# Performance work log

Measured on AMD Instinct MI355X. Metric: run time of the kernel, lower is better.

The kernel has to match this reference:

```python
import jax, jax.numpy as jnp
import numpy as np

N_NODES = 100000
N_EDGES = 1600000
HEADS = 8
CH = 16
NEG_SLOPE = 0.2


def setup_inputs() -> dict:
    key = jax.random.key(0)
    ks = jax.random.split(key, 8)
    x = jax.random.normal(ks[0], (N_NODES, 16), dtype=jnp.float32)
    edge_index = jax.random.randint(ks[1], (2, N_EDGES), 0, N_NODES, dtype=jnp.int64)
    W = jax.random.normal(ks[2], (16, HEADS * CH), dtype=jnp.float32) * 0.25
    att_src = jax.random.normal(ks[3], (HEADS, CH), dtype=jnp.float32) * 0.25
    att_dst = jax.random.normal(ks[4], (HEADS, CH), dtype=jnp.float32) * 0.25
    bias = jax.random.normal(ks[5], (HEADS * CH,), dtype=jnp.float32) * 0.1
    fc_w = jax.random.normal(ks[6], (HEADS * CH, 5), dtype=jnp.float32) * 0.1
    fc_b = jax.random.normal(ks[7], (5,), dtype=jnp.float32) * 0.1
    return {"x": x, "edge_index": edge_index, "W": W, "att_src": att_src,
            "att_dst": att_dst, "bias": bias, "fc_w": fc_w, "fc_b": fc_b}


def reference(x, edge_index, W, att_src, att_dst, bias, fc_w, fc_b):
    N = x.shape[0]
    # PyG GATConv default: add self loops
    loops = jnp.arange(N, dtype=edge_index.dtype)
    src = jnp.concatenate([edge_index[0], loops])
    dst = jnp.concatenate([edge_index[1], loops])

    h = (x @ W).reshape(N, HEADS, CH)                 # [N,H,C]
    a_src = jnp.einsum('nhc,hc->nh', h, att_src)      # [N,H]
    a_dst = jnp.einsum('nhc,hc->nh', h, att_dst)      # [N,H]

    e = a_src[src] + a_dst[dst]                       # [E,H]
    e = jax.nn.leaky_relu(e, NEG_SLOPE)
    # segment softmax over edges grouped by destination node
    e_max = jax.ops.segment_max(e, dst, num_segments=N)
    e_exp = jnp.exp(e - e_max[dst])
    denom = jax.ops.segment_sum(e_exp, dst, num_segments=N)
    alpha = e_exp / (denom[dst] + 1e-16)              # [E,H]

    msg = alpha[:, :, None] * h[src]                  # [E,H,C]
    out = jax.ops.segment_sum(msg, dst, num_segments=N)  # [N,H,C]
    out = out.reshape(N, HEADS * CH) + bias           # concat heads + bias

    out = jax.nn.relu(out)
    # dropout is identity in eval mode
    logits = out @ fc_w + fc_b                        # [N,5]
    return jax.nn.log_softmax(logits, axis=1)
```

## Files before the change

kernel.cpp:

```cpp
#include <hip/hip_runtime.h>
#include <hip/hip_bf16.h>
#include <hip/hip_fp16.h>
#include <math.h>

#define N_NODES 100000
#define N_EDGES 1600000
#define HEADS 8
#define HC 128
#define LOG2E 1.44269504f

#define DPB 64
#define NB 1563
#define NBP (NB + 1)
#define NCH 512
#define EPC (N_EDGES / NCH)
#define CAPS 1664
#define WSTR (CAPS + 4)
#define NA 196

__global__ __launch_bounds__(512) void k_prep(
    const float* __restrict__ x, const float* __restrict__ W,
    const float* __restrict__ att_s, const float* __restrict__ att_d,
    const int* __restrict__ ei,
    unsigned short* __restrict__ a_srcb, float* __restrict__ a_dst,
    uint4* __restrict__ x2b,
    int* __restrict__ offs, unsigned* __restrict__ stg) {
    __shared__ int smem[2048 + EPC];
    __shared__ int ws8[8];
    int t = threadIdx.x;
    if (blockIdx.x >= NCH) {
        float* sM = (float*)smem;
        if (t < 256) {
            int k = t >> 4, h2 = t & 15;
            const float* av = (h2 < 8) ? att_s : att_d;
            int h = h2 & 7;
            float s = 0.f;
#pragma unroll
            for (int c = 0; c < 16; ++c)
                s = fmaf(W[k * HC + h * 16 + c], av[h * 16 + c], s);
            sM[k * 16 + h2] = s * LOG2E;
        }
        __syncthreads();
        int node = (blockIdx.x - NCH) * 512 + t;
        if (node < N_NODES) {
            const float4* xr = (const float4*)(x + node * 16);
            float4 x0 = xr[0], x1 = xr[1], x2 = xr[2], x3 = xr[3];
            float xv[16] = {x0.x, x0.y, x0.z, x0.w, x1.x, x1.y, x1.z, x1.w,
                            x2.x, x2.y, x2.z, x2.w, x3.x, x3.y, x3.z, x3.w};
            union { uint4 u[2]; __hip_bfloat162 b[8]; } px;
#pragma unroll
            for (int k = 0; k < 8; ++k)
                px.b[k] = __float22bfloat162_rn(float2{xv[2 * k], xv[2 * k + 1]});
            x2b[node * 2] = px.u[0];
            x2b[node * 2 + 1] = px.u[1];
#pragma unroll
            for (int h2 = 0; h2 < 16; ++h2) {
                float o = 0.f;
#pragma unroll
                for (int k = 0; k < 16; ++k) o = fmaf(xv[k], sM[k * 16 + h2], o);
                if (h2 < 8) a_srcb[node * 8 + h2] =
                    __bfloat16_as_ushort(__float2bfloat16(o));
                else        a_dst[node * 8 + (h2 - 8)] = o;
            }
        }
    } else {
        int* hist = smem;
        unsigned* entries = (unsigned*)(smem + 2048);
        int c = blockIdx.x;
        hist[t] = 0; hist[t + 512] = 0; hist[t + 1024] = 0; hist[t + 1536] = 0;
        __syncthreads();
        int beg = c * EPC, end = beg + EPC;
        for (int e = beg + t; e < end; e += 512)
            atomicAdd(&hist[ei[N_EDGES + e] >> 6], 1);
        __syncthreads();
        int i0 = 4 * t;
        int v0 = hist[i0], v1 = hist[i0 + 1], v2 = hist[i0 + 2], v3 = hist[i0 + 3];
        int s1 = v0 + v1, s2 = s1 + v2, T = s2 + v3;
        int lane = t & 63, wv = t >> 6;
        int inc = T;
#pragma unroll
        for (int off = 1; off < 64; off <<= 1) {
            int y = __shfl_up(inc, off);
            if (lane >= off) inc += y;
        }
        if (lane == 63) ws8[wv] = inc;
        __syncthreads();
        int wbase = 0;
        for (int k = 0; k < wv; ++k) wbase += ws8[k];
        int e0 = wbase + inc - T;
        hist[i0] = e0; hist[i0 + 1] = e0 + v0;
        hist[i0 + 2] = e0 + s1; hist[i0 + 3] = e0 + s2;
        __syncthreads();
        int row = c * NBP;
        for (int b = t; b < NB; b += 512) offs[row + b] = hist[b];
        if (t == 0) offs[row + NB] = EPC;
        __syncthreads();
        for (int e = beg + t; e < end; e += 512) {
            int src = ei[e], dst = ei[N_EDGES + e];
            int pos = atomicAdd(&hist[dst >> 6], 1);
            entries[pos] = ((unsigned)(dst & 63) << 17) | (unsigned)src;
        }
        __syncthreads();
        unsigned* so = stg + beg;
        for (int i = t; i < EPC; i += 512) so[i] = entries[i];
    }
}

__global__ __launch_bounds__(256) void k_tr(const int* __restrict__ offs,
                                            int* __restrict__ offsT) {
    __shared__ int tile[64][65];
    int b0 = (blockIdx.x >> 3) * 64;
    int c0 = (blockIdx.x & 7) * 64;
    int t = threadIdx.x;
    for (int i = t; i < 4096; i += 256) {
        int cc = i >> 6, bb = i & 63;
        int b = b0 + bb;
        tile[bb][cc] = (b < NBP) ? offs[(c0 + cc) * NBP + b] : 0;
    }
    __syncthreads();
    for (int i = t; i < 4096; i += 256) {
        int bb = i >> 6, cc = i & 63;
        int b = b0 + bb;
        if (b < NBP) offsT[b * NCH + c0 + cc] = tile[bb][cc];
    }
}

__global__ __launch_bounds__(512) void k_gather(
    const __hip_bfloat162* __restrict__ x2b,
    const unsigned short* __restrict__ a_srcb, const float* __restrict__ W,
    const float* __restrict__ a_dst,
    const int* __restrict__ offsT, const unsigned* __restrict__ stg,
    const float* __restrict__ bias, const float* __restrict__ fc_w,
    const float* __restrict__ fc_b, float* __restrict__ out) {
    __shared__ __align__(16) unsigned buf0[(8 * WSTR) / 2];
    __shared__ __align__(16) int cstage[CAPS];
    __shared__ __align__(16) float sW[16 * HC];
    __shared__ int o0_s[NCH];
    __shared__ int myb_s[NCH + 1];
    __shared__ __align__(16) float sad[8 * DPB + 8];
    __shared__ int hist[DPB];
    __shared__ int bs[DPB + 1];
    __shared__ int ws8[8];
    unsigned* estage = buf0;
    unsigned short* wst = (unsigned short*)buf0;
    int b = blockIdx.x, t = threadIdx.x;
    int d0 = b * DPB;
    for (int i = t; i < 16 * HC; i += 512) sW[i] = W[i];
    sad[t] = (d0 * 8 + t < N_NODES * 8) ? a_dst[(size_t)d0 * 8 + t] : 0.f;
    if (t < 8) sad[8 * DPB + t] = -100000.f;
    int lane = t & 63, wv = t >> 6;
    {
        int o0 = offsT[b * NCH + t];
        int len = offsT[(b + 1) * NCH + t] - o0;
        o0_s[t] = o0;
        int inc = len;
#pragma unroll
        for (int off = 1; off < 64; off <<= 1) {
            int y = __shfl_up(inc, off);
            if (lane >= off) inc += y;
        }
        if (lane == 63) ws8[wv] = inc;
        __syncthreads();
        int wbase = 0;
        for (int k = 0; k < wv; ++k) wbase += ws8[k];
        myb_s[t] = wbase + inc - len;
        if (t == 511) myb_s[NCH] = wbase + inc;
    }
    if (t < DPB) hist[t] = (d0 + t < N_NODES) ? 1 : 0;
    __syncthreads();
    int tot = myb_s[NCH];
    for (int i = t; i < tot; i += 512) {
        int lo = 0, hi = NCH - 1;
#pragma unroll
        for (int s = 0; s < 9; ++s) {
            int mid = (lo + hi + 1) >> 1;
            if (myb_s[mid] <= i) lo = mid; else hi = mid - 1;
        }
        estage[i] = stg[lo * EPC + o0_s[lo] + (i - myb_s[lo])];
    }
    __syncthreads();
    for (int i = t; i < tot; i += 512) atomicAdd(&hist[estage[i] >> 17], 1);
    __syncthreads();
    if (t < 64) {
        int gd = d0 + t;
        bool val = gd < N_NODES;
        int len = hist[t];
        int plen = (len + 3) & ~3;
        int iv = plen;
#pragma unroll
        for (int off = 1; off < 64; off <<= 1) {
            int y = __shfl_up(iv, off);
            if (t >= off) iv += y;
        }
        int excl = iv - plen;
        bs[t] = excl;
        if (t == 63) bs[64] = iv;
        if (val) cstage[excl] = (t << 17) | gd;
        hist[t] = excl + (val ? 1 : 0);
        for (int k = len; k < plen; ++k) cstage[excl + k] = (64 << 17);
    }
    __syncthreads();
    for (int i = t; i < tot; i += 512) {
        unsigned u = estage[i];
        int pos = atomicAdd(&hist[u >> 17], 1);
        cstage[pos] = (int)u;
    }
    __syncthreads();
    int ctot = bs[DPB];
    for (int i = t; i < ctot; i += 512) {
        unsigned u = (unsigned)cstage[i];
        int s = (int)(u & 0x1FFFF);
        int dl = (int)(u >> 17);
        union { uint4 v; __hip_bfloat162 b2[4]; } pa;
        pa.v = *(const uint4*)(a_srcb + (size_t)s * 8);
        const float* adp = sad + dl * 8;
        float4 ad0 = *(const float4*)(adp);
        float4 ad1 = *(const float4*)(adp + 4);
        float2 s01 = __bfloat1622float2(pa.b2[0]);
        float2 s23 = __bfloat1622float2(pa.b2[1]);
        float2 s45 = __bfloat1622float2(pa.b2[2]);
        float2 s67 = __bfloat1622float2(pa.b2[3]);
        float e[8] = {s01.x + ad0.x, s01.y + ad0.y, s23.x + ad0.z, s23.y + ad0.w,
                      s45.x + ad1.x, s45.y + ad1.y, s67.x + ad1.z, s67.y + ad1.w};
#pragma unroll
        for (int h = 0; h < 8; ++h) {
            float eh = fmaxf(e[h], 0.2f * e[h]);
            float w = exp2f(eh);
            wst[h * WSTR + i] = __half_as_ushort(__float2half(w));
        }
    }
    __syncthreads();
    int q = t & 15, g = t >> 4;
    int head = q >> 1, i8 = q & 1;
    int c0 = head * 16 + i8 * 8;
    const unsigned short* wrow = wst + head * WSTR;
    int xofs = i8 * 16;
    const char* xb = (const char*)x2b;
    float bb[8], fwv[8][5], fbv[5];
#pragma unroll
    for (int m = 0; m < 8; ++m) bb[m] = bias[c0 + m];
#pragma unroll
    for (int m = 0; m < 8; ++m)
#pragma unroll
        for (int jj = 0; jj < 5; ++jj) fwv[m][jj] = fc_w[(c0 + m) * 5 + jj];
#pragma unroll
    for (int jj = 0; jj < 5; ++jj) fbv[jj] = fc_b[jj];
    for (int l4 = 0; l4 < 2; ++l4) {
        int l = g * 2 + l4;
        int gd = d0 + l;
        if (gd >= N_NODES) break;
        int beg = bs[l], end = bs[l + 1];
        float A[8] = {0.f, 0.f, 0.f, 0.f, 0.f, 0.f, 0.f, 0.f};
        float wsum = 0.f;
        auto acc = [&](const uint4& xv, float w) {
            union { uint4 v; __hip_bfloat162 b2[4]; } xx; xx.v = xv;
            float2 f0 = __bfloat1622float2(xx.b2[0]);
            float2 f1 = __bfloat1622float2(xx.b2[1]);
            float2 f2 = __bfloat1622float2(xx.b2[2]);
            float2 f3 = __bfloat1622float2(xx.b2[3]);
            A[0] = fmaf(w, f0.x, A[0]); A[1] = fmaf(w, f0.y, A[1]);
            A[2] = fmaf(w, f1.x, A[2]); A[3] = fmaf(w, f1.y, A[3]);
            A[4] = fmaf(w, f2.x, A[4]); A[5] = fmaf(w, f2.y, A[5]);
            A[6] = fmaf(w, f3.x, A[6]); A[7] = fmaf(w, f3.y, A[7]);
        };
        for (int j = beg; j < end; j += 4) {
            int4 cs = *(const int4*)(cstage + j);
            uint2 wu = *(const uint2*)(wrow + j);
            union { uint2 u2; __half2 h2[2]; } wq; wq.u2 = wu;
            float2 w01 = __half22float2(wq.h2[0]);
            float2 w23 = __half22float2(wq.h2[1]);
            int s0 = cs.x & 0x1FFFF, s1 = cs.y & 0x1FFFF;
            int s2 = cs.z & 0x1FFFF, s3 = cs.w & 0x1FFFF;
            uint4 xv0 = *(const uint4*)(xb + ((s0 << 5) + xofs));
            uint4 xv1 = *(const uint4*)(xb + ((s1 << 5) + xofs));
            uint4 xv2 = *(const uint4*)(xb + ((s2 << 5) + xofs));
            uint4 xv3 = *(const uint4*)(xb + ((s3 << 5) + xofs));
            acc(xv0, w01.x); acc(xv1, w01.y);
            acc(xv2, w23.x); acc(xv3, w23.y);
            wsum += (w01.x + w01.y) + (w23.x + w23.y);
        }
        float inv = 1.f / (wsum + 1e-16f);
#pragma unroll
        for (int m = 0; m < 8; ++m) A[m] *= inv;
        float ov[8] = {0.f, 0.f, 0.f, 0.f, 0.f, 0.f, 0.f, 0.f};
#pragma unroll
        for (int m = 0; m < 8; ++m) {
            float a = A[m];
            float ap = __shfl_xor(A[m], 1);
            const float* w0r = sW + (i8 * 8 + m) * HC + c0;
            const float* w1r = sW + ((1 - i8) * 8 + m) * HC + c0;
#pragma unroll
            for (int o = 0; o < 8; ++o) ov[o] = fmaf(a, w0r[o], ov[o]);
#pragma unroll
            for (int o = 0; o < 8; ++o) ov[o] = fmaf(ap, w1r[o], ov[o]);
        }
#pragma unroll
        for (int m = 0; m < 8; ++m) ov[m] = fmaxf(ov[m] + bb[m], 0.f);
        float p[5];
#pragma unroll
        for (int jj = 0; jj < 5; ++jj) {
            float sacc = 0.f;
#pragma unroll
            for (int m = 0; m < 8; ++m) sacc = fmaf(ov[m], fwv[m][jj], sacc);
            p[jj] = sacc;
        }
#pragma unroll
        for (int off = 8; off >= 1; off >>= 1)
#pragma unroll
            for (int jj = 0; jj < 5; ++jj) p[jj] += __shfl_xor(p[jj], off);
        if (q == 0) {
            float lg[5], mx = -1e30f;
#pragma unroll
            for (int jj = 0; jj < 5; ++jj) {
                lg[jj] = p[jj] + fbv[jj];
                mx = fmaxf(mx, lg[jj]);
            }
            float sum = 0.f;
#pragma unroll
            for (int jj = 0; jj < 5; ++jj) sum += __expf(lg[jj] - mx);
            float ls = mx + __logf(sum);
#pragma unroll
            for (int jj = 0; jj < 5; ++jj) out[gd * 5 + jj] = lg[jj] - ls;
        }
    }
}

extern "C" void kernel_launch(void* const* d_in, const int* in_sizes, int n_in,
                              void* d_out, int out_size, void* d_ws, size_t ws_size,
                              hipStream_t stream) {
    const float* x     = (const float*)d_in[0];
    const int*   ei    = (const int*)d_in[1];
    const float* W     = (const float*)d_in[2];
    const float* att_s = (const float*)d_in[3];
    const float* att_d = (const float*)d_in[4];
    const float* bias  = (const float*)d_in[5];
    const float* fc_w  = (const float*)d_in[6];
    const float* fc_b  = (const float*)d_in[7];
    float* out = (float*)d_out;

    char* ws = (char*)d_ws;
    size_t off = 0;
    auto carve = [&](size_t bytes) {
        void* p = ws + off;
        off = (off + bytes + 255) & ~(size_t)255;
        return p;
    };
    unsigned short* a_srcb = (unsigned short*)carve((size_t)N_NODES * HEADS * 2);
    float*    a_dst = (float*)   carve((size_t)N_NODES * HEADS * 4);
    uint4*    x2b   = (uint4*)   carve((size_t)N_NODES * 32);
    int*      offs  = (int*)     carve((size_t)NCH * NBP * 4);
    int*      offsT = (int*)     carve((size_t)NBP * NCH * 4);
    unsigned* stg   = (unsigned*)carve((size_t)N_EDGES * 4);

    k_prep<<<NCH + NA, 512, 0, stream>>>(x, W, att_s, att_d, ei,
                                         a_srcb, a_dst, x2b, offs, stg);
    k_tr<<<200, 256, 0, stream>>>(offs, offsT);
    k_gather<<<NB, 512, 0, stream>>>((const __hip_bfloat162*)x2b, a_srcb, W,
                                     a_dst, offsT, stg, bias, fc_w, fc_b, out);
}
```

Before: 166.4 us.

## Balance per-node gather work by sorted degree pairing and software-pipeline loads

```diff
diff --git a/kernel.cpp b/kernel.cpp
--- a/kernel.cpp
+++ b/kernel.cpp
@@ -70,8 +70,13 @@
         hist[t] = 0; hist[t + 512] = 0; hist[t + 1024] = 0; hist[t + 1536] = 0;
         __syncthreads();
         int beg = c * EPC, end = beg + EPC;
-        for (int e = beg + t; e < end; e += 512)
-            atomicAdd(&hist[ei[N_EDGES + e] >> 6], 1);
+        int dsh[7];
+#pragma unroll
+        for (int k = 0; k < 7; ++k) {
+            int ee = beg + t + k * 512;
+            dsh[k] = (ee < end) ? ei[N_EDGES + ee] : -1;
+            if (dsh[k] >= 0) atomicAdd(&hist[dsh[k] >> 6], 1);
+        }
         __syncthreads();
         int i0 = 4 * t;
         int v0 = hist[i0], v1 = hist[i0 + 1], v2 = hist[i0 + 2], v3 = hist[i0 + 3];
@@ -95,10 +100,14 @@
         for (int b = t; b < NB; b += 512) offs[row + b] = hist[b];
         if (t == 0) offs[row + NB] = EPC;
         __syncthreads();
-        for (int e = beg + t; e < end; e += 512) {
-            int src = ei[e], dst = ei[N_EDGES + e];
-            int pos = atomicAdd(&hist[dst >> 6], 1);
-            entries[pos] = ((unsigned)(dst & 63) << 17) | (unsigned)src;
+#pragma unroll
+        for (int k = 0; k < 7; ++k) {
+            int ee = beg + t + k * 512;
+            if (dsh[k] >= 0) {
+                int src = ei[ee];
+                int pos = atomicAdd(&hist[dsh[k] >> 6], 1);
+                entries[pos] = ((unsigned)(dsh[k] & 63) << 17) | (unsigned)src;
+            }
         }
         __syncthreads();
         unsigned* so = stg + beg;
@@ -140,6 +149,7 @@
     __shared__ __align__(16) float sad[8 * DPB + 8];
     __shared__ int hist[DPB];
     __shared__ int bs[DPB + 1];
+    __shared__ int rord[DPB];
     __shared__ int ws8[8];
     unsigned* estage = buf0;
     unsigned short* wst = (unsigned short*)buf0;
@@ -198,6 +208,19 @@
         if (val) cstage[excl] = (t << 17) | gd;
         hist[t] = excl + (val ? 1 : 0);
         for (int k = len; k < plen; ++k) cstage[excl + k] = (64 << 17);
+        int key = (plen << 6) | t;
+#pragma unroll
+        for (int k = 2; k <= 64; k <<= 1) {
+#pragma unroll
+            for (int jj = k >> 1; jj >= 1; jj >>= 1) {
+                int partner = __shfl_xor(key, jj);
+                bool up = ((t & k) == 0);
+                bool takeMax = (((t & jj) != 0) == up);
+                key = takeMax ? (key > partner ? key : partner)
+                              : (key < partner ? key : partner);
+            }
+        }
+        rord[t] = key & 63;
     }
     __syncthreads();
     for (int i = t; i < tot; i += 512) {
@@ -246,9 +269,9 @@
 #pragma unroll
     for (int jj = 0; jj < 5; ++jj) fbv[jj] = fc_b[jj];
     for (int l4 = 0; l4 < 2; ++l4) {
-        int l = g * 2 + l4;
+        int l = rord[l4 == 0 ? g : 63 - g];
         int gd = d0 + l;
-        if (gd >= N_NODES) break;
+        if (gd >= N_NODES) continue;
         int beg = bs[l], end = bs[l + 1];
         float A[8] = {0.f, 0.f, 0.f, 0.f, 0.f, 0.f, 0.f, 0.f};
         float wsum = 0.f;
@@ -263,18 +286,32 @@
             A[4] = fmaf(w, f2.x, A[4]); A[5] = fmaf(w, f2.y, A[5]);
             A[6] = fmaf(w, f3.x, A[6]); A[7] = fmaf(w, f3.y, A[7]);
         };
-        for (int j = beg; j < end; j += 4) {
-            int4 cs = *(const int4*)(cstage + j);
-            uint2 wu = *(const uint2*)(wrow + j);
+        if (beg < end) {
+            int4 cs = *(const int4*)(cstage + beg);
+            uint2 wu = *(const uint2*)(wrow + beg);
+            uint4 xv0 = *(const uint4*)(xb + (((cs.x & 0x1FFFF) << 5) + xofs));
+            uint4 xv1 = *(const uint4*)(xb + (((cs.y & 0x1FFFF) << 5) + xofs));
+            uint4 xv2 = *(const uint4*)(xb + (((cs.z & 0x1FFFF) << 5) + xofs));
+            uint4 xv3 = *(const uint4*)(xb + (((cs.w & 0x1FFFF) << 5) + xofs));
+            for (int j = beg + 4; j < end; j += 4) {
+                int4 csn = *(const int4*)(cstage + j);
+                uint2 wun = *(const uint2*)(wrow + j);
+                uint4 nx0 = *(const uint4*)(xb + (((csn.x & 0x1FFFF) << 5) + xofs));
+                uint4 nx1 = *(const uint4*)(xb + (((csn.y & 0x1FFFF) << 5) + xofs));
+                uint4 nx2 = *(const uint4*)(xb + (((csn.z & 0x1FFFF) << 5) + xofs));
+                uint4 nx3 = *(const uint4*)(xb + (((csn.w & 0x1FFFF) << 5) + xofs));
+                union { uint2 u2; __half2 h2[2]; } wq; wq.u2 = wu;
+                float2 w01 = __half22float2(wq.h2[0]);
+                float2 w23 = __half22float2(wq.h2[1]);
+                acc(xv0, w01.x); acc(xv1, w01.y);
+                acc(xv2, w23.x); acc(xv3, w23.y);
+                wsum += (w01.x + w01.y) + (w23.x + w23.y);
+                cs = csn; wu = wun;
+                xv0 = nx0; xv1 = nx1; xv2 = nx2; xv3 = nx3;
+            }
             union { uint2 u2; __half2 h2[2]; } wq; wq.u2 = wu;
             float2 w01 = __half22float2(wq.h2[0]);
             float2 w23 = __half22float2(wq.h2[1]);
-            int s0 = cs.x & 0x1FFFF, s1 = cs.y & 0x1FFFF;
-            int s2 = cs.z & 0x1FFFF, s3 = cs.w & 0x1FFFF;
-            uint4 xv0 = *(const uint4*)(xb + ((s0 << 5) + xofs));
-            uint4 xv1 = *(const uint4*)(xb + ((s1 << 5) + xofs));
-            uint4 xv2 = *(const uint4*)(xb + ((s2 << 5) + xofs));
-            uint4 xv3 = *(const uint4*)(xb + ((s3 << 5) + xofs));
             acc(xv0, w01.x); acc(xv1, w01.y);
             acc(xv2, w23.x); acc(xv3, w23.y);
             wsum += (w01.x + w01.y) + (w23.x + w23.y);
```

Measured after the change: 196.8 us. 1.18x slower.

## Cut gather LDS footprint, read W from global, register-cache dst in binning

Applied to the files above, without the earlier changes.

```diff
diff --git a/kernel.cpp b/kernel.cpp
--- a/kernel.cpp
+++ b/kernel.cpp
@@ -70,8 +70,13 @@
         hist[t] = 0; hist[t + 512] = 0; hist[t + 1024] = 0; hist[t + 1536] = 0;
         __syncthreads();
         int beg = c * EPC, end = beg + EPC;
-        for (int e = beg + t; e < end; e += 512)
-            atomicAdd(&hist[ei[N_EDGES + e] >> 6], 1);
+        int dsh[7];
+#pragma unroll
+        for (int k = 0; k < 7; ++k) {
+            int ee = beg + t + k * 512;
+            dsh[k] = (ee < end) ? ei[N_EDGES + ee] : -1;
+            if (dsh[k] >= 0) atomicAdd(&hist[dsh[k] >> 6], 1);
+        }
         __syncthreads();
         int i0 = 4 * t;
         int v0 = hist[i0], v1 = hist[i0 + 1], v2 = hist[i0 + 2], v3 = hist[i0 + 3];
@@ -95,10 +100,14 @@
         for (int b = t; b < NB; b += 512) offs[row + b] = hist[b];
         if (t == 0) offs[row + NB] = EPC;
         __syncthreads();
-        for (int e = beg + t; e < end; e += 512) {
-            int src = ei[e], dst = ei[N_EDGES + e];
-            int pos = atomicAdd(&hist[dst >> 6], 1);
-            entries[pos] = ((unsigned)(dst & 63) << 17) | (unsigned)src;
+#pragma unroll
+        for (int k = 0; k < 7; ++k) {
+            int ee = beg + t + k * 512;
+            if (dsh[k] >= 0) {
+                int src = ei[ee];
+                int pos = atomicAdd(&hist[dsh[k] >> 6], 1);
+                entries[pos] = ((unsigned)(dsh[k] & 63) << 17) | (unsigned)src;
+            }
         }
         __syncthreads();
         unsigned* so = stg + beg;
@@ -125,7 +134,7 @@
     }
 }
 
-__global__ __launch_bounds__(512) void k_gather(
+__global__ __launch_bounds__(512, 8) void k_gather(
     const __hip_bfloat162* __restrict__ x2b,
     const unsigned short* __restrict__ a_srcb, const float* __restrict__ W,
     const float* __restrict__ a_dst,
@@ -133,19 +142,18 @@
     const float* __restrict__ bias, const float* __restrict__ fc_w,
     const float* __restrict__ fc_b, float* __restrict__ out) {
     __shared__ __align__(16) unsigned buf0[(8 * WSTR) / 2];
-    __shared__ __align__(16) int cstage[CAPS];
-    __shared__ __align__(16) float sW[16 * HC];
-    __shared__ int o0_s[NCH];
-    __shared__ int myb_s[NCH + 1];
+    __shared__ __align__(16) int sbuf[CAPS];
     __shared__ __align__(16) float sad[8 * DPB + 8];
     __shared__ int hist[DPB];
     __shared__ int bs[DPB + 1];
     __shared__ int ws8[8];
     unsigned* estage = buf0;
     unsigned short* wst = (unsigned short*)buf0;
+    int* cstage = sbuf;
+    int* o0_s = sbuf;
+    int* myb_s = sbuf + 512;
     int b = blockIdx.x, t = threadIdx.x;
     int d0 = b * DPB;
-    for (int i = t; i < 16 * HC; i += 512) sW[i] = W[i];
     sad[t] = (d0 * 8 + t < N_NODES * 8) ? a_dst[(size_t)d0 * 8 + t] : 0.f;
     if (t < 8) sad[8 * DPB + t] = -100000.f;
     int lane = t & 63, wv = t >> 6;
@@ -287,8 +295,8 @@
         for (int m = 0; m < 8; ++m) {
             float a = A[m];
             float ap = __shfl_xor(A[m], 1);
-            const float* w0r = sW + (i8 * 8 + m) * HC + c0;
-            const float* w1r = sW + ((1 - i8) * 8 + m) * HC + c0;
+            const float* w0r = W + (i8 * 8 + m) * HC + c0;
+            const float* w1r = W + ((1 - i8) * 8 + m) * HC + c0;
 #pragma unroll
             for (int o = 0; o < 8; ++o) ov[o] = fmaf(a, w0r[o], ov[o]);
 #pragma unroll
```

Result: slower. 252.7 us (+51.9%).
